# Kernel optimization log

Hardware: AMD Instinct MI355X
Metric: run time of the kernel (lower is better)

The kernel has to match this reference:

```python
import jax, jax.numpy as jnp
import numpy as np

INF = 1000000000000000.0  # 1e15, matches the TF source

B, H, S, D = 4, 16, 1024, 64


def setup_inputs() -> dict:
    key = jax.random.key(0)
    kq, kk, kv, kp = jax.random.split(key, 4)
    q = jax.random.normal(kq, (B, H, S, D), dtype=jnp.float32)
    k = jax.random.normal(kk, (B, H, S, D), dtype=jnp.float32)
    v = jax.random.normal(kv, (B, H, S, D), dtype=jnp.float32)
    # pad_mask: 1 = masked-out key position, broadcast over heads and queries
    pad_mask = jax.random.randint(kp, (B, 1, 1, S), 0, 2, dtype=jnp.int32)
    # look_ahead_mask: 1 above the diagonal (future positions masked)
    look_ahead_mask = jnp.triu(jnp.ones((S, S), dtype=jnp.int32), k=1)[None, None]
    return {"q": q, "k": k, "v": v, "pad_mask": pad_mask,
            "look_ahead_mask": look_ahead_mask}


def reference(q, k, v, pad_mask, look_ahead_mask):
    d_model = jnp.float32(q.shape[3])
    # scores: (B, H, Sq, Sk)
    score_logits = jnp.einsum("bhqd,bhkd->bhqk", q, k) / jnp.sqrt(d_model)
    if pad_mask is not None:
        score_logits = score_logits + pad_mask.astype(jnp.float32) * (-INF)
    if look_ahead_mask is not None:
        score_logits = score_logits + look_ahead_mask.astype(jnp.float32) * (-INF)
    attention_weights = jax.nn.softmax(score_logits, axis=-1)
    context_vector = jnp.einsum("bhqk,bhkd->bhqd", attention_weights, v)
    return (context_vector, attention_weights)
```

## Files before the change

### kernel.cpp

```cpp
#include <hip/hip_runtime.h>
#include <stdint.h>

#define S 1024
#define D 64
#define TQ 16
#define KT 128
#define NKT 8
#define NEG (-1e15f)
#define SCALE 0.125f

#define WB_STRIDE 1048
#define QS_STRIDE 72

typedef __bf16 bf16x8 __attribute__((ext_vector_type(8)));
typedef float f32x4 __attribute__((ext_vector_type(4)));
typedef unsigned short ushort_t;

__device__ __forceinline__ unsigned short f2b(float f) {
  union { float f; uint32_t u; } c; c.f = f;
  uint32_t u = c.u;
  return (unsigned short)((u + 0x7fffu + ((u >> 16) & 1u)) >> 16);
}
__device__ __forceinline__ float b2f(uint32_t u) {
  union { uint32_t u; float f; } c; c.u = u << 16;
  return c.f;
}

__device__ __forceinline__ void barrier_lds_only() {
  asm volatile("s_waitcnt lgkmcnt(0)" ::: "memory");
  __builtin_amdgcn_s_barrier();
  __builtin_amdgcn_sched_barrier(0);
}

__global__ __launch_bounds__(256) void prep_k_kernel(
    const float* __restrict__ Kg, ushort_t* __restrict__ Kb)
{
  const size_t idx = ((size_t)blockIdx.x * 256 + threadIdx.x) * 8;
  float4 a = *(const float4*)(Kg + idx);
  float4 b = *(const float4*)(Kg + idx + 4);
  ushort_t tmp[8];
  tmp[0]=f2b(a.x); tmp[1]=f2b(a.y); tmp[2]=f2b(a.z); tmp[3]=f2b(a.w);
  tmp[4]=f2b(b.x); tmp[5]=f2b(b.y); tmp[6]=f2b(b.z); tmp[7]=f2b(b.w);
  *(uint4*)(Kb + idx) = *(const uint4*)tmp;
}

__global__ __launch_bounds__(256) void prep_vt_kernel(
    const float* __restrict__ Vg, ushort_t* __restrict__ Vt)
{
  __shared__ __align__(16) ushort_t lvt[D * QS_STRIDE];
  const int t = threadIdx.x;
  const int bh = blockIdx.x >> 4;
  const int j0 = (blockIdx.x & 15) << 6;

  {
    const int j = t >> 2, sd = (t & 3) << 4;
    const float* src = Vg + ((size_t)bh * S + j0 + j) * D + sd;
#pragma unroll
    for (int c = 0; c < 4; ++c) {
      float4 f = *(const float4*)(src + (c << 2));
      lvt[(sd + (c << 2) + 0) * QS_STRIDE + j] = f2b(f.x);
      lvt[(sd + (c << 2) + 1) * QS_STRIDE + j] = f2b(f.y);
      lvt[(sd + (c << 2) + 2) * QS_STRIDE + j] = f2b(f.z);
      lvt[(sd + (c << 2) + 3) * QS_STRIDE + j] = f2b(f.w);
    }
  }
  __syncthreads();
  {
    const int d = t >> 2, sj = (t & 3) << 4;
    ushort_t tmp[16];
#pragma unroll
    for (int c = 0; c < 4; ++c)
      *(ushort4*)&tmp[c << 2] = *(const ushort4*)&lvt[d * QS_STRIDE + sj + (c << 2)];
    ushort_t* dst = Vt + ((size_t)bh * D + d) * S + j0 + sj;
    *(uint4*)dst = *(const uint4*)&tmp[0];
    *(uint4*)(dst + 8) = *(const uint4*)&tmp[8];
  }
}

__global__ __launch_bounds__(512, 4) void attn_kernel(
    const float* __restrict__ Qg, const ushort_t* __restrict__ Kb,
    const ushort_t* __restrict__ Vtb, const int* __restrict__ PADg,
    float* __restrict__ OCTX, float* __restrict__ OW)
{
  __shared__ __align__(16) ushort_t wb[TQ * WB_STRIDE];

  const int t  = threadIdx.x;
  const int w  = t >> 6;
  const int l  = t & 63;
  const int la = l & 15;
  const int lb = l >> 4;

  const int hwblk = blockIdx.x;
  const int slot  = hwblk >> 3;
  const int bh    = ((hwblk & 7) << 3) + (slot >> 6);
  const int qt    = slot & 63;
  const int qr0   = qt << 4;

  const size_t head = (size_t)bh * S * D;
  const int* pp = PADg + (size_t)(bh >> 4) * S;

  float padf[16];
#pragma unroll
  for (int ii = 0; ii < 8; ++ii) {
    const int j = (l << 1) + (ii << 7);
    int2 pv = *(const int2*)&pp[j];
    padf[2 * ii]     = pv.x ? NEG : 0.0f;
    padf[2 * ii + 1] = pv.y ? NEG : 0.0f;
  }

  bf16x8 aq0, aq1;
  {
    const float* qrow = Qg + head + (size_t)(qr0 + la) * D + (lb << 3);
    float4 q00 = *(const float4*)(qrow);
    float4 q01 = *(const float4*)(qrow + 4);
    float4 q10 = *(const float4*)(qrow + 32);
    float4 q11 = *(const float4*)(qrow + 36);
    ushort_t a0[8], a1[8];
    a0[0]=f2b(q00.x); a0[1]=f2b(q00.y); a0[2]=f2b(q00.z); a0[3]=f2b(q00.w);
    a0[4]=f2b(q01.x); a0[5]=f2b(q01.y); a0[6]=f2b(q01.z); a0[7]=f2b(q01.w);
    a1[0]=f2b(q10.x); a1[1]=f2b(q10.y); a1[2]=f2b(q10.z); a1[3]=f2b(q10.w);
    a1[4]=f2b(q11.x); a1[5]=f2b(q11.y); a1[6]=f2b(q11.z); a1[7]=f2b(q11.w);
    aq0 = *(const bf16x8*)a0;
    aq1 = *(const bf16x8*)a1;
  }

  {
    const ushort_t* kbase = Kb + head + (size_t)((w << 4) + la) * D + (lb << 3);
    bf16x8 kf[16];
#pragma unroll
    for (int st = 0; st < 16; ++st)
      kf[st] = *(const bf16x8*)(kbase + (size_t)(st >> 1) * (KT * D) + (st & 1) * 32);
    __builtin_amdgcn_sched_barrier(0);
#pragma unroll
    for (int kt = 0; kt < NKT; ++kt) {
      f32x4 acc = {0.f, 0.f, 0.f, 0.f};
      acc = __builtin_amdgcn_mfma_f32_16x16x32_bf16(aq0, kf[2 * kt],     acc, 0, 0, 0);
      acc = __builtin_amdgcn_mfma_f32_16x16x32_bf16(aq1, kf[2 * kt + 1], acc, 0, 0, 0);
#pragma unroll
      for (int i = 0; i < 4; ++i)
        wb[((lb << 2) + i) * WB_STRIDE + kt * KT + (w << 4) + la] = f2b(acc[i]);
    }
  }
  __syncthreads();

  const int jh = w >> 2;
  const int d0 = (w & 3) << 4;
  const ushort_t* vrow = Vtb + (size_t)bh * (D * S) + (size_t)(d0 + la) * S
                        + jh * 64 + (lb << 3);
  bf16x8 vf[16];
#pragma unroll
  for (int st = 0; st < 16; ++st)
    vf[st] = *(const bf16x8*)(vrow + (st >> 1) * KT + (st & 1) * 32);
  __builtin_amdgcn_sched_barrier(0);

#pragma unroll
  for (int rr = 0; rr < 2; ++rr) {
    const int r  = (w << 1) + rr;
    const int qr = qr0 + r;
    float lg[16];
    float m = -3.0e38f;
#pragma unroll
    for (int ii = 0; ii < 8; ++ii) {
      const int j = (l << 1) + (ii << 7);
      uint32_t pr = *(const uint32_t*)&wb[r * WB_STRIDE + j];
      float l0 = b2f(pr & 0xffffu) * SCALE + padf[2 * ii]     + ((j     > qr) ? NEG : 0.0f);
      float l1 = b2f(pr >> 16)     * SCALE + padf[2 * ii + 1] + ((j + 1 > qr) ? NEG : 0.0f);
      lg[2 * ii] = l0; lg[2 * ii + 1] = l1;
      m = fmaxf(m, fmaxf(l0, l1));
    }
#pragma unroll
    for (int off = 32; off > 0; off >>= 1) m = fmaxf(m, __shfl_xor(m, off, 64));
    float sum = 0.f;
#pragma unroll
    for (int x = 0; x < 16; ++x) { lg[x] = __expf(lg[x] - m); sum += lg[x]; }
#pragma unroll
    for (int off = 32; off > 0; off >>= 1) sum += __shfl_xor(sum, off, 64);
    const float inv = 1.0f / sum;
    float* orow = OW + (size_t)(bh * S + qr) * S;
#pragma unroll
    for (int ii = 0; ii < 8; ++ii) {
      const int j = (l << 1) + (ii << 7);
      float w0 = lg[2 * ii] * inv, w1 = lg[2 * ii + 1] * inv;
      *(uint32_t*)&wb[r * WB_STRIDE + j] = ((uint32_t)f2b(w1) << 16) | (uint32_t)f2b(w0);
      unsigned long long uw = ((unsigned long long)__float_as_uint(w1) << 32)
                            | (unsigned long long)__float_as_uint(w0);
      __builtin_nontemporal_store(uw, (unsigned long long*)&orow[j]);
    }
  }
  barrier_lds_only();

  f32x4 cacc;
  {
    const ushort_t* wrow = &wb[la * WB_STRIDE + jh * 64 + (lb << 3)];
    f32x4 ca = {0.f, 0.f, 0.f, 0.f}, cb = {0.f, 0.f, 0.f, 0.f};
#pragma unroll
    for (int st = 0; st < 16; ++st) {
      bf16x8 av = *(const bf16x8*)(wrow + (st >> 1) * KT + (st & 1) * 32);
      if (st & 1) cb = __builtin_amdgcn_mfma_f32_16x16x32_bf16(av, vf[st], cb, 0, 0, 0);
      else        ca = __builtin_amdgcn_mfma_f32_16x16x32_bf16(av, vf[st], ca, 0, 0, 0);
    }
    cacc = ca + cb;
  }
  barrier_lds_only();

  float* pbuf = (float*)wb;
  if (w >= 4) {
#pragma unroll
    for (int i = 0; i < 4; ++i)
      pbuf[(w - 4) * 320 + ((lb << 2) + i) * 20 + la] = cacc[i];
  }
  barrier_lds_only();
  if (w < 4) {
#pragma unroll
    for (int i = 0; i < 4; ++i) {
      const int qrow = (lb << 2) + i;
      __builtin_nontemporal_store(
          cacc[i] + pbuf[w * 320 + qrow * 20 + la],
          &OCTX[((size_t)(bh * S) + qr0 + qrow) * D + d0 + la]);
    }
  }
}

extern "C" void kernel_launch(void* const* d_in, const int* in_sizes, int n_in,
                              void* d_out, int out_size, void* d_ws, size_t ws_size,
                              hipStream_t stream) {
  const float* q   = (const float*)d_in[0];
  const float* k   = (const float*)d_in[1];
  const float* v   = (const float*)d_in[2];
  const int*   pad = (const int*)d_in[3];
  float* ctx  = (float*)d_out;
  float* wout = (float*)d_out + (size_t)4 * 16 * S * D;

  ushort_t* Kb  = (ushort_t*)d_ws;
  ushort_t* Vtb = (ushort_t*)d_ws + (size_t)4 * 16 * S * D;

  prep_k_kernel <<<dim3(2048), dim3(256), 0, stream>>>(k, Kb);
  prep_vt_kernel<<<dim3(1024), dim3(256), 0, stream>>>(v, Vtb);
  attn_kernel   <<<dim3(4096), dim3(512), 0, stream>>>(q, Kb, Vtb, pad, ctx, wout);
}
```

Baseline: 436.3 us.

## Cut register pressure with double-buffered K/V fragment loads to raise occupancy

Replaces the up-front preload of all 16 K and 16 V fragments into registers with a two-deep rolling prefetch. Pad mask values are now reloaded inside the softmax loop instead of being held in registers. Launch bounds rise from 4 to 6 blocks per CU, and a separate LDS buffer for the partial context sums removes one barrier. The aim is higher occupancy to hide latency, at the cost of exposing more global load latency inside the MFMA loops and issuing extra pad loads.

```diff
diff --git a/kernel.cpp b/kernel.cpp
--- a/kernel.cpp
+++ b/kernel.cpp
@@ -77,12 +77,13 @@
   }
 }
 
-__global__ __launch_bounds__(512, 4) void attn_kernel(
+__global__ __launch_bounds__(512, 6) void attn_kernel(
     const float* __restrict__ Qg, const ushort_t* __restrict__ Kb,
     const ushort_t* __restrict__ Vtb, const int* __restrict__ PADg,
     float* __restrict__ OCTX, float* __restrict__ OW)
 {
   __shared__ __align__(16) ushort_t wb[TQ * WB_STRIDE];
+  __shared__ __align__(16) float pbuf[4 * 320];
 
   const int t  = threadIdx.x;
   const int w  = t >> 6;
@@ -98,15 +99,6 @@
 
   const size_t head = (size_t)bh * S * D;
   const int* pp = PADg + (size_t)(bh >> 4) * S;
-
-  float padf[16];
-#pragma unroll
-  for (int ii = 0; ii < 8; ++ii) {
-    const int j = (l << 1) + (ii << 7);
-    int2 pv = *(const int2*)&pp[j];
-    padf[2 * ii]     = pv.x ? NEG : 0.0f;
-    padf[2 * ii + 1] = pv.y ? NEG : 0.0f;
-  }
 
   bf16x8 aq0, aq1;
   {
@@ -126,31 +118,37 @@
 
   {
     const ushort_t* kbase = Kb + head + (size_t)((w << 4) + la) * D + (lb << 3);
-    bf16x8 kf[16];
-#pragma unroll
-    for (int st = 0; st < 16; ++st)
-      kf[st] = *(const bf16x8*)(kbase + (size_t)(st >> 1) * (KT * D) + (st & 1) * 32);
-    __builtin_amdgcn_sched_barrier(0);
+    const int j0 = w << 4;
+    bf16x8 k0[2], k1[2];
+    k0[0] = *(const bf16x8*)(kbase);
+    k1[0] = *(const bf16x8*)(kbase + 32);
+    k0[1] = *(const bf16x8*)(kbase + (size_t)(KT * D));
+    k1[1] = *(const bf16x8*)(kbase + (size_t)(KT * D) + 32);
 #pragma unroll
     for (int kt = 0; kt < NKT; ++kt) {
+      bf16x8 c0 = k0[kt & 1], c1 = k1[kt & 1];
+      if (kt + 2 < NKT) {
+        const ushort_t* ns = kbase + (size_t)(kt + 2) * (KT * D);
+        k0[kt & 1] = *(const bf16x8*)(ns);
+        k1[kt & 1] = *(const bf16x8*)(ns + 32);
+      }
       f32x4 acc = {0.f, 0.f, 0.f, 0.f};
-      acc = __builtin_amdgcn_mfma_f32_16x16x32_bf16(aq0, kf[2 * kt],     acc, 0, 0, 0);
-      acc = __builtin_amdgcn_mfma_f32_16x16x32_bf16(aq1, kf[2 * kt + 1], acc, 0, 0, 0);
+      acc = __builtin_amdgcn_mfma_f32_16x16x32_bf16(aq0, c0, acc, 0, 0, 0);
+      acc = __builtin_amdgcn_mfma_f32_16x16x32_bf16(aq1, c1, acc, 0, 0, 0);
 #pragma unroll
       for (int i = 0; i < 4; ++i)
-        wb[((lb << 2) + i) * WB_STRIDE + kt * KT + (w << 4) + la] = f2b(acc[i]);
-    }
-  }
-  __syncthreads();
+        wb[((lb << 2) + i) * WB_STRIDE + kt * KT + j0 + la] = f2b(acc[i]);
+    }
+  }
+  barrier_lds_only();
 
   const int jh = w >> 2;
   const int d0 = (w & 3) << 4;
-  const ushort_t* vrow = Vtb + (size_t)bh * (D * S) + (size_t)(d0 + la) * S
+  const ushort_t* vbase = Vtb + (size_t)bh * (D * S) + (size_t)(d0 + la) * S
                         + jh * 64 + (lb << 3);
-  bf16x8 vf[16];
-#pragma unroll
-  for (int st = 0; st < 16; ++st)
-    vf[st] = *(const bf16x8*)(vrow + (st >> 1) * KT + (st & 1) * 32);
+  bf16x8 vv[2];
+  vv[0] = *(const bf16x8*)(vbase);
+  vv[1] = *(const bf16x8*)(vbase + 32);
   __builtin_amdgcn_sched_barrier(0);
 
 #pragma unroll
@@ -163,8 +161,9 @@
     for (int ii = 0; ii < 8; ++ii) {
       const int j = (l << 1) + (ii << 7);
       uint32_t pr = *(const uint32_t*)&wb[r * WB_STRIDE + j];
-      float l0 = b2f(pr & 0xffffu) * SCALE + padf[2 * ii]     + ((j     > qr) ? NEG : 0.0f);
-      float l1 = b2f(pr >> 16)     * SCALE + padf[2 * ii + 1] + ((j + 1 > qr) ? NEG : 0.0f);
+      int2 pv = *(const int2*)&pp[j];
+      float l0 = b2f(pr & 0xffffu) * SCALE + (pv.x ? NEG : 0.0f) + ((j     > qr) ? NEG : 0.0f);
+      float l1 = b2f(pr >> 16)     * SCALE + (pv.y ? NEG : 0.0f) + ((j + 1 > qr) ? NEG : 0.0f);
       lg[2 * ii] = l0; lg[2 * ii + 1] = l1;
       m = fmaxf(m, fmaxf(l0, l1));
     }
@@ -195,15 +194,18 @@
     f32x4 ca = {0.f, 0.f, 0.f, 0.f}, cb = {0.f, 0.f, 0.f, 0.f};
 #pragma unroll
     for (int st = 0; st < 16; ++st) {
-      bf16x8 av = *(const bf16x8*)(wrow + (st >> 1) * KT + (st & 1) * 32);
-      if (st & 1) cb = __builtin_amdgcn_mfma_f32_16x16x32_bf16(av, vf[st], cb, 0, 0, 0);
-      else        ca = __builtin_amdgcn_mfma_f32_16x16x32_bf16(av, vf[st], ca, 0, 0, 0);
+      bf16x8 bv = vv[st & 1];
+      if (st + 2 < 16) {
+        const int sn = st + 2;
+        vv[st & 1] = *(const bf16x8*)(vbase + (sn >> 1) * KT + (sn & 1) * 32);
+      }
+      bf16x8 af = *(const bf16x8*)(wrow + (st >> 1) * KT + (st & 1) * 32);
+      if (st & 1) cb = __builtin_amdgcn_mfma_f32_16x16x32_bf16(af, bv, cb, 0, 0, 0);
+      else        ca = __builtin_amdgcn_mfma_f32_16x16x32_bf16(af, bv, ca, 0, 0, 0);
     }
     cacc = ca + cb;
   }
-  barrier_lds_only();
-
-  float* pbuf = (float*)wb;
+
   if (w >= 4) {
 #pragma unroll
     for (int i = 0; i < 4; ++i)
```

New measurement: 442.1 us. Within noise of the previous version (+1.3%).
